# Performance work log

Hardware: AMD Instinct MI355X
Metric: run time of the kernel (lower is better)

## Reference

```python
import jax, jax.numpy as jnp
import numpy as np

B, C, H, W = 8, 256, 128, 128
K = 3                      # kernel_size
GC = 16                    # group_channels
G = C // GC                # groups = 16
RED = 4                    # reduction_ratio (hardcoded in module)
CR = C // RED              # 64
PAD = (K - 1) // 2


def setup_inputs() -> dict:
    key = jax.random.key(0)
    ks = jax.random.split(key, 8)
    s = 0.05
    return {
        "x":  jax.random.normal(ks[0], (B, C, H, W), dtype=jnp.float32),
        # conv1[0]: 1x1 Conv2d(C, C//4)
        "w1": jax.random.normal(ks[1], (CR, C), dtype=jnp.float32) * s,
        "b1": jax.random.normal(ks[2], (CR,), dtype=jnp.float32) * s,
        # conv1[1]: depthwise KxK Conv2d(C//4, C//4, groups=C//4), padding=K//2
        "wd": jax.random.normal(ks[3], (CR, 1, K, K), dtype=jnp.float32) * s,
        "bd": jax.random.normal(ks[4], (CR,), dtype=jnp.float32) * s,
        # conv2: 1x1 Conv2d(C//4, K*K*G)
        "w2": jax.random.normal(ks[5], (K * K * G, CR), dtype=jnp.float32) * s,
        "b2": jax.random.normal(ks[6], (K * K * G,), dtype=jnp.float32) * s,
    }


def _forward(x, w1, b1, wd, bd, w2, b2):
    # weight generation branch: 1x1 conv -> depthwise KxK conv -> 1x1 conv
    y = jnp.einsum("oc,bchw->bohw", w1, x) + b1[None, :, None, None]
    y = jax.lax.conv_general_dilated(
        y, wd, window_strides=(1, 1),
        padding=[(PAD, PAD), (PAD, PAD)],
        feature_group_count=CR,
        dimension_numbers=("NCHW", "OIHW", "NCHW"),
    ) + bd[None, :, None, None]
    w = jnp.einsum("oc,bchw->bohw", w2, y) + b2[None, :, None, None]
    w = w.reshape(B, G, K, K, H, W)  # per-pixel dynamic depthwise weights

    # involution-style per-pixel depthwise conv, stride=1, padding=(K-1)//2
    xr = x.reshape(B, G, GC, H, W)
    xp = jnp.pad(xr, ((0, 0), (0, 0), (0, 0), (PAD, PAD), (PAD, PAD)))
    out = jnp.zeros((B, G, GC, H, W), dtype=x.dtype)
    for kh in range(K):          # small fixed structural loop (K*K = 9 taps)
        for kw in range(K):
            out = out + xp[:, :, :, kh:kh + H, kw:kw + W] * w[:, :, kh, kw][:, :, None, :, :]
    return out.reshape(B, C, H, W)


def reference(x, w1, b1, wd, bd, w2, b2):
    return _forward(x, w1, b1, wd, bd, w2, b2)
```

## Files before the change

kernel.cpp:

```cpp
#include <hip/hip_runtime.h>
#include <hip/hip_bf16.h>

#define HW    16384
#define IMW   128
#define IMH   128
#define CIN   256
#define CR    64
#define G     16
#define GC    16

typedef __attribute__((ext_vector_type(8))) short short8;
typedef __attribute__((ext_vector_type(4))) float floatx4;

static __device__ __forceinline__ short f2bf(float f) {
  union { float f; unsigned u; } v; v.f = f;
  unsigned r = v.u + 0x7fffu + ((v.u >> 16) & 1u);
  return (short)(r >> 16);
}
static __device__ __forceinline__ float bf2f(short s) {
  union { unsigned u; float f; } v; v.u = ((unsigned)(unsigned short)s) << 16;
  return v.f;
}

__global__ __launch_bounds__(256) void k_cvt_w1(const float* __restrict__ w1,
                                                short* __restrict__ w1b) {
  const int i = blockIdx.x * 256 + threadIdx.x;
  w1b[i] = f2bf(w1[i]);
}

__global__ __launch_bounds__(256) void k_conv1_mfma(const float* __restrict__ x,
                                                    const short* __restrict__ w1b,
                                                    const float* __restrict__ b1,
                                                    short* __restrict__ y1b) {
  const int blk  = blockIdx.x;
  const int b    = blk >> 8;
  const int pt   = blk & 255;
  const int wave = threadIdx.x >> 6;
  const int lane = threadIdx.x & 63;
  const int quad = lane >> 4;
  const int l16  = lane & 15;
  const int p    = pt * 64 + wave * 16 + l16;

  const float* xb = x + (size_t)b * CIN * HW + p;

  floatx4 acc[4];
#pragma unroll
  for (int mt = 0; mt < 4; ++mt)
#pragma unroll
    for (int r = 0; r < 4; ++r) acc[mt][r] = b1[mt * 16 + quad * 4 + r];

#pragma unroll 1
  for (int kk = 0; kk < CIN; kk += 64) {
    short8 af0[4], af1[4];
#pragma unroll
    for (int mt = 0; mt < 4; ++mt) {
      af0[mt] = *(const short8*)(w1b + (mt * 16 + l16) * CIN + kk + quad * 8);
      af1[mt] = *(const short8*)(w1b + (mt * 16 + l16) * CIN + kk + 32 + quad * 8);
    }
    float xv0[8], xv1[8];
#pragma unroll
    for (int j = 0; j < 8; ++j)
      xv0[j] = xb[(size_t)(kk + quad * 8 + j) * HW];
#pragma unroll
    for (int j = 0; j < 8; ++j)
      xv1[j] = xb[(size_t)(kk + 32 + quad * 8 + j) * HW];

    short8 bf0, bf1;
#pragma unroll
    for (int j = 0; j < 8; ++j) bf0[j] = f2bf(xv0[j]);
#pragma unroll
    for (int j = 0; j < 8; ++j) bf1[j] = f2bf(xv1[j]);

#pragma unroll
    for (int mt = 0; mt < 4; ++mt)
      acc[mt] = __builtin_amdgcn_mfma_f32_16x16x32_bf16(af0[mt], bf0, acc[mt], 0, 0, 0);
#pragma unroll
    for (int mt = 0; mt < 4; ++mt)
      acc[mt] = __builtin_amdgcn_mfma_f32_16x16x32_bf16(af1[mt], bf1, acc[mt], 0, 0, 0);
  }

  short* yb = y1b + (size_t)b * CR * HW + p;
#pragma unroll
  for (int mt = 0; mt < 4; ++mt)
#pragma unroll
    for (int r = 0; r < 4; ++r)
      yb[(size_t)(mt * 16 + quad * 4 + r) * HW] = f2bf(acc[mt][r]);
}

__global__ __launch_bounds__(256) void k_dw(const short* __restrict__ y1b,
                                            const float* __restrict__ wd,
                                            const float* __restrict__ bd,
                                            short* __restrict__ y2b) {
  const int blk   = blockIdx.x;
  const int strip = blk & 3;
  const int c     = (blk >> 2) & 63;
  const int b     = blk >> 8;
  const int tcol  = threadIdx.x & 15;
  const int trow  = threadIdx.x >> 4;
  const int r0    = strip * 32 + trow * 2;
  const int c0    = tcol * 8;

  const short* src = y1b + (size_t)(b * CR + c) * HW;

  const float mcl = c0 > 0 ? 1.f : 0.f;
  const float mcr = c0 + 8 < IMW ? 1.f : 0.f;
  const int   cl  = c0 > 0 ? c0 - 1 : 0;
  const int   crr = c0 + 8 < IMW ? c0 + 8 : IMW - 1;

  float f[4][10];
#pragma unroll
  for (int i = 0; i < 4; ++i) {
    const int rr = r0 - 1 + i;
    const int rc = rr < 0 ? 0 : (rr > IMH - 1 ? IMH - 1 : rr);
    const float mr = (rr < 0 || rr > IMH - 1) ? 0.f : 1.f;
    const short* row = src + rc * IMW;
    const short8 v = *(const short8*)(row + c0);
#pragma unroll
    for (int j = 0; j < 8; ++j) f[i][j + 1] = mr * bf2f(v[j]);
    f[i][0] = mr * mcl * bf2f(row[cl]);
    f[i][9] = mr * mcr * bf2f(row[crr]);
  }

  float wv[9];
#pragma unroll
  for (int j = 0; j < 9; ++j) wv[j] = wd[c * 9 + j];
  const float bias = bd[c];

  short* dst = y2b + (size_t)(b * CR + c) * HW + r0 * IMW + c0;
#pragma unroll
  for (int i = 0; i < 2; ++i) {
    short8 o;
#pragma unroll
    for (int xcol = 0; xcol < 8; ++xcol) {
      float acc = bias;
#pragma unroll
      for (int kh = 0; kh < 3; ++kh)
#pragma unroll
        for (int kw = 0; kw < 3; ++kw)
          acc += wv[kh * 3 + kw] * f[i + kh][xcol + kw];
      o[xcol] = f2bf(acc);
    }
    *(short8*)(dst + i * IMW) = o;
  }
}

__global__ __launch_bounds__(256) void k_conv2invol(const float* __restrict__ x,
                                                    const short* __restrict__ y2b,
                                                    const float* __restrict__ w2,
                                                    const float* __restrict__ b2,
                                                    float* __restrict__ out) {
  const int blk  = blockIdx.x;
  const int tile = blk & 63;
  const int gp   = (blk >> 6) & 7;
  const int b    = blk >> 9;
  const int g0   = gp * 2;
  const int tid  = threadIdx.x;
  const int tr   = tid >> 5;
  const int tc   = tid & 31;
  const int h    = (tile >> 2) * 8 + tr;
  const int w    = (tile & 3) * 32 + tc;
  const int p    = h * IMW + w;

  float wv[2][9];
#pragma unroll
  for (int q = 0; q < 2; ++q)
#pragma unroll
    for (int j = 0; j < 9; ++j) wv[q][j] = b2[(g0 + q) * 9 + j];

  const short* y2p = y2b + (size_t)b * CR * HW + p;
#pragma unroll 2
  for (int c = 0; c < CR; c += 4) {
    const float v0 = bf2f(y2p[(size_t)(c + 0) * HW]);
    const float v1 = bf2f(y2p[(size_t)(c + 1) * HW]);
    const float v2 = bf2f(y2p[(size_t)(c + 2) * HW]);
    const float v3 = bf2f(y2p[(size_t)(c + 3) * HW]);
#pragma unroll
    for (int q = 0; q < 2; ++q)
#pragma unroll
      for (int j = 0; j < 9; ++j) {
        const float4 wq = *(const float4*)(w2 + ((g0 + q) * 9 + j) * CR + c);
        wv[q][j] += wq.x * v0 + wq.y * v1 + wq.z * v2 + wq.w * v3;
      }
  }

  const int   hcl[3] = {h > 0 ? h - 1 : 0, h, h < IMH - 1 ? h + 1 : IMH - 1};
  const int   wcl[3] = {w > 0 ? w - 1 : 0, w, w < IMW - 1 ? w + 1 : IMW - 1};
  const float mr[3]  = {h > 0 ? 1.f : 0.f, 1.f, h < IMH - 1 ? 1.f : 0.f};
  const float mc[3]  = {w > 0 ? 1.f : 0.f, 1.f, w < IMW - 1 ? 1.f : 0.f};
  int rel[9];
#pragma unroll
  for (int kh = 0; kh < 3; ++kh)
#pragma unroll
    for (int kw = 0; kw < 3; ++kw) {
      rel[kh * 3 + kw] = hcl[kh] * IMW + wcl[kw];
      const float m = mr[kh] * mc[kw];
      wv[0][kh * 3 + kw] *= m;
      wv[1][kh * 3 + kw] *= m;
    }

  const float* xb = x + (size_t)b * CIN * HW;
  float*       ob = out + (size_t)b * CIN * HW;

#pragma unroll
  for (int q = 0; q < 2; ++q) {
#pragma unroll 4
    for (int cc = 0; cc < GC; ++cc) {
      const int ch = (g0 + q) * GC + cc;
      const float* xp = xb + (size_t)ch * HW;
      float acc = 0.f;
#pragma unroll
      for (int j = 0; j < 9; ++j) acc += wv[q][j] * xp[rel[j]];
      ob[(size_t)ch * HW + p] = acc;
    }
  }
}

extern "C" void kernel_launch(void* const* d_in, const int* in_sizes, int n_in,
                              void* d_out, int out_size, void* d_ws, size_t ws_size,
                              hipStream_t stream) {
  const float* x  = (const float*)d_in[0];
  const float* w1 = (const float*)d_in[1];
  const float* b1 = (const float*)d_in[2];
  const float* wd = (const float*)d_in[3];
  const float* bd = (const float*)d_in[4];
  const float* w2 = (const float*)d_in[5];
  const float* b2 = (const float*)d_in[6];
  float* out = (float*)d_out;

  short* w1b = (short*)d_ws;
  short* y1b = (short*)((char*)d_ws + 65536);
  short* y2b = y1b + (size_t)8 * CR * HW;

  k_cvt_w1<<<dim3(64), dim3(256), 0, stream>>>(w1, w1b);
  k_conv1_mfma<<<dim3(2048), dim3(256), 0, stream>>>(x, w1b, b1, y1b);
  k_dw<<<dim3(2048), dim3(256), 0, stream>>>(y1b, wd, bd, y2b);
  k_conv2invol<<<dim3(4096), dim3(256), 0, stream>>>(x, y2b, w2, b2, out);
}
```

Measured before the change: 353.3 us.

## Generate involution weights with split-bf16 MFMA and vectorize the involution stage

The per-pixel weight generation (the conv2 1x1 projection) now runs on bf16 MFMA instead of scalar FMAs. w2 is split into a high and a residual bf16 part to keep accuracy close to fp32. Each block computes 144x64 weights into shared memory and then applies the 3x3 involution to all 16 groups for a 64-pixel row segment, with each thread handling 4 contiguous pixels through float4 loads and stores. This removes the redundant weight recomputation the old layout did per group pair and cuts scalar load traffic. In exchange it doubles the MFMA count and adds shared memory and a barrier per block. The bf16 w1 buffer is now aliased onto the y2 buffer, which is safe only because conv1 finishes reading it before the depthwise kernel writes y2.

```diff
diff --git a/kernel.cpp b/kernel.cpp
--- a/kernel.cpp
+++ b/kernel.cpp
@@ -8,6 +8,7 @@
 #define CR    64
 #define G     16
 #define GC    16
+#define M2    144
 
 typedef __attribute__((ext_vector_type(8))) short short8;
 typedef __attribute__((ext_vector_type(4))) float floatx4;
@@ -22,10 +23,22 @@
   return v.f;
 }
 
-__global__ __launch_bounds__(256) void k_cvt_w1(const float* __restrict__ w1,
-                                                short* __restrict__ w1b) {
-  const int i = blockIdx.x * 256 + threadIdx.x;
-  w1b[i] = f2bf(w1[i]);
+__global__ __launch_bounds__(256) void k_cvt(const float* __restrict__ w1,
+                                             const float* __restrict__ w2,
+                                             short* __restrict__ w1b,
+                                             short* __restrict__ w2b,
+                                             short* __restrict__ w2r) {
+  const int blk = blockIdx.x;
+  if (blk < 64) {
+    const int i = blk * 256 + threadIdx.x;
+    w1b[i] = f2bf(w1[i]);
+  } else {
+    const int i = (blk - 64) * 256 + threadIdx.x;
+    const float v = w2[i];
+    const short hb = f2bf(v);
+    w2b[i] = hb;
+    w2r[i] = f2bf(v - bf2f(hb));
+  }
 }
 
 __global__ __launch_bounds__(256) void k_conv1_mfma(const float* __restrict__ x,
@@ -144,74 +157,116 @@
   }
 }
 
-__global__ __launch_bounds__(256) void k_conv2invol(const float* __restrict__ x,
+__global__ __launch_bounds__(256) void k_wgen_invol(const float* __restrict__ x,
                                                     const short* __restrict__ y2b,
-                                                    const float* __restrict__ w2,
+                                                    const short* __restrict__ w2b,
+                                                    const short* __restrict__ w2r,
                                                     const float* __restrict__ b2,
                                                     float* __restrict__ out) {
+  __shared__ float wgt[M2 * 64];
   const int blk  = blockIdx.x;
-  const int tile = blk & 63;
-  const int gp   = (blk >> 6) & 7;
-  const int b    = blk >> 9;
-  const int g0   = gp * 2;
+  const int b    = blk >> 8;
+  const int pt   = blk & 255;
   const int tid  = threadIdx.x;
-  const int tr   = tid >> 5;
-  const int tc   = tid & 31;
-  const int h    = (tile >> 2) * 8 + tr;
-  const int w    = (tile & 3) * 32 + tc;
-  const int p    = h * IMW + w;
-
-  float wv[2][9];
-#pragma unroll
-  for (int q = 0; q < 2; ++q)
-#pragma unroll
-    for (int j = 0; j < 9; ++j) wv[q][j] = b2[(g0 + q) * 9 + j];
-
-  const short* y2p = y2b + (size_t)b * CR * HW + p;
+  const int wave = tid >> 6;
+  const int lane = tid & 63;
+  const int quad = lane >> 4;
+  const int l16  = lane & 15;
+
+  {
+    const int p = pt * 64 + wave * 16 + l16;
+    const short* y2p = y2b + (size_t)b * CR * HW + p;
+
+    floatx4 acc[9];
+#pragma unroll
+    for (int mt = 0; mt < 9; ++mt)
+#pragma unroll
+      for (int r = 0; r < 4; ++r) acc[mt][r] = b2[mt * 16 + quad * 4 + r];
+
+#pragma unroll
+    for (int kk = 0; kk < CR; kk += 32) {
+      short8 bfrag;
+#pragma unroll
+      for (int j = 0; j < 8; ++j)
+        bfrag[j] = y2p[(size_t)(kk + quad * 8 + j) * HW];
+#pragma unroll
+      for (int mt = 0; mt < 9; ++mt) {
+        const short8 af = *(const short8*)(w2b + (mt * 16 + l16) * CR + kk + quad * 8);
+        acc[mt] = __builtin_amdgcn_mfma_f32_16x16x32_bf16(af, bfrag, acc[mt], 0, 0, 0);
+      }
+#pragma unroll
+      for (int mt = 0; mt < 9; ++mt) {
+        const short8 ar = *(const short8*)(w2r + (mt * 16 + l16) * CR + kk + quad * 8);
+        acc[mt] = __builtin_amdgcn_mfma_f32_16x16x32_bf16(ar, bfrag, acc[mt], 0, 0, 0);
+      }
+    }
+
+#pragma unroll
+    for (int mt = 0; mt < 9; ++mt)
+#pragma unroll
+      for (int r = 0; r < 4; ++r)
+        wgt[(mt * 16 + quad * 4 + r) * 64 + wave * 16 + l16] = acc[mt][r];
+  }
+  __syncthreads();
+
+  const int pq  = tid & 15;
+  const int g   = tid >> 4;
+  const int h   = pt >> 1;
+  const int c0q = (pt & 1) * 64 + pq * 4;
+  const int p0  = h * IMW + c0q;
+
+  float wv[9][4];
+#pragma unroll
+  for (int j = 0; j < 9; ++j) {
+    const float4 v = *(const float4*)&wgt[(g * 9 + j) * 64 + pq * 4];
+    wv[j][0] = v.x; wv[j][1] = v.y; wv[j][2] = v.z; wv[j][3] = v.w;
+  }
+
+  if (h == 0) {
+#pragma unroll
+    for (int j = 0; j < 3; ++j)
+      wv[j][0] = wv[j][1] = wv[j][2] = wv[j][3] = 0.f;
+  }
+  if (h == IMH - 1) {
+#pragma unroll
+    for (int j = 6; j < 9; ++j)
+      wv[j][0] = wv[j][1] = wv[j][2] = wv[j][3] = 0.f;
+  }
+  if (c0q == 0)       { wv[0][0] = wv[3][0] = wv[6][0] = 0.f; }
+  if (c0q == IMW - 4) { wv[2][3] = wv[5][3] = wv[8][3] = 0.f; }
+
+  const int r[3] = { (h > 0 ? h - 1 : 0) * IMW, h * IMW,
+                     (h < IMH - 1 ? h + 1 : IMH - 1) * IMW };
+  const int cl = c0q > 0 ? c0q - 1 : 0;
+  const int cr = c0q + 4 < IMW ? c0q + 4 : IMW - 1;
+
+  const float* xg = x   + ((size_t)b * CIN + (size_t)g * GC) * HW;
+  float*       og = out + ((size_t)b * CIN + (size_t)g * GC) * HW;
+
 #pragma unroll 2
-  for (int c = 0; c < CR; c += 4) {
-    const float v0 = bf2f(y2p[(size_t)(c + 0) * HW]);
-    const float v1 = bf2f(y2p[(size_t)(c + 1) * HW]);
-    const float v2 = bf2f(y2p[(size_t)(c + 2) * HW]);
-    const float v3 = bf2f(y2p[(size_t)(c + 3) * HW]);
-#pragma unroll
-    for (int q = 0; q < 2; ++q)
-#pragma unroll
-      for (int j = 0; j < 9; ++j) {
-        const float4 wq = *(const float4*)(w2 + ((g0 + q) * 9 + j) * CR + c);
-        wv[q][j] += wq.x * v0 + wq.y * v1 + wq.z * v2 + wq.w * v3;
-      }
-  }
-
-  const int   hcl[3] = {h > 0 ? h - 1 : 0, h, h < IMH - 1 ? h + 1 : IMH - 1};
-  const int   wcl[3] = {w > 0 ? w - 1 : 0, w, w < IMW - 1 ? w + 1 : IMW - 1};
-  const float mr[3]  = {h > 0 ? 1.f : 0.f, 1.f, h < IMH - 1 ? 1.f : 0.f};
-  const float mc[3]  = {w > 0 ? 1.f : 0.f, 1.f, w < IMW - 1 ? 1.f : 0.f};
-  int rel[9];
-#pragma unroll
-  for (int kh = 0; kh < 3; ++kh)
-#pragma unroll
-    for (int kw = 0; kw < 3; ++kw) {
-      rel[kh * 3 + kw] = hcl[kh] * IMW + wcl[kw];
-      const float m = mr[kh] * mc[kw];
-      wv[0][kh * 3 + kw] *= m;
-      wv[1][kh * 3 + kw] *= m;
-    }
-
-  const float* xb = x + (size_t)b * CIN * HW;
-  float*       ob = out + (size_t)b * CIN * HW;
-
-#pragma unroll
-  for (int q = 0; q < 2; ++q) {
-#pragma unroll 4
-    for (int cc = 0; cc < GC; ++cc) {
-      const int ch = (g0 + q) * GC + cc;
-      const float* xp = xb + (size_t)ch * HW;
+  for (int cc = 0; cc < GC; ++cc) {
+    const float* xp = xg + (size_t)cc * HW;
+    float v[3][6];
+#pragma unroll
+    for (int rr = 0; rr < 3; ++rr) {
+      const float4 m = *(const float4*)(xp + r[rr] + c0q);
+      v[rr][0] = xp[r[rr] + cl];
+      v[rr][1] = m.x; v[rr][2] = m.y; v[rr][3] = m.z; v[rr][4] = m.w;
+      v[rr][5] = xp[r[rr] + cr];
+    }
+    float o[4];
+#pragma unroll
+    for (int px = 0; px < 4; ++px) {
       float acc = 0.f;
 #pragma unroll
-      for (int j = 0; j < 9; ++j) acc += wv[q][j] * xp[rel[j]];
-      ob[(size_t)ch * HW + p] = acc;
-    }
+      for (int kh = 0; kh < 3; ++kh)
+#pragma unroll
+        for (int kw = 0; kw < 3; ++kw)
+          acc += wv[kh * 3 + kw][px] * v[kh][px + kw];
+      o[px] = acc;
+    }
+    float4 ov; ov.x = o[0]; ov.y = o[1]; ov.z = o[2]; ov.w = o[3];
+    *(float4*)(og + (size_t)cc * HW + p0) = ov;
   }
 }
 
@@ -227,12 +282,14 @@
   const float* b2 = (const float*)d_in[6];
   float* out = (float*)d_out;
 
-  short* w1b = (short*)d_ws;
-  short* y1b = (short*)((char*)d_ws + 65536);
-  short* y2b = y1b + (size_t)8 * CR * HW;
-
-  k_cvt_w1<<<dim3(64), dim3(256), 0, stream>>>(w1, w1b);
+  short* w2b = (short*)d_ws;
+  short* w2r = (short*)((char*)d_ws + 18432);
+  short* y1b = (short*)((char*)d_ws + 36864);
+  short* y2b = (short*)((char*)d_ws + 16814080);
+  short* w1b = y2b;
+
+  k_cvt<<<dim3(100), dim3(256), 0, stream>>>(w1, w2, w1b, w2b, w2r);
   k_conv1_mfma<<<dim3(2048), dim3(256), 0, stream>>>(x, w1b, b1, y1b);
   k_dw<<<dim3(2048), dim3(256), 0, stream>>>(y1b, wd, bd, y2b);
-  k_conv2invol<<<dim3(4096), dim3(256), 0, stream>>>(x, y2b, w2, b2, out);
-}
+  k_wgen_invol<<<dim3(2048), dim3(256), 0, stream>>>(x, y2b, w2b, w2r, b2, out);
+}
```

New measurement: 403.4 us. 14.2% more time.

## Compute conv2 dynamic weights with bf16 MFMA using split hi/lo weights

Applied to the files above, without the earlier changes.

Replaces the scalar FMA loop that produced the 18 per-pixel involution weights with bf16 MFMA tiles. w2 is pre-packed into a padded bf16 high part plus a bf16 residual so precision stays close to fp32. Results go through shared memory to the per-pixel involution stage. This removes redundant w2 loads and scalar FMAs, at the cost of a __syncthreads, 18KB of LDS per block, wasted MFMA rows from padding 18 to 32, and uncoalesced short gathers of y2b. w1b now aliases the y2b workspace region, which is safe because it is consumed by conv1 before k_dw writes y2b.

```diff
diff --git a/kernel.cpp b/kernel.cpp
--- a/kernel.cpp
+++ b/kernel.cpp
@@ -22,10 +22,25 @@
   return v.f;
 }
 
-__global__ __launch_bounds__(256) void k_cvt_w1(const float* __restrict__ w1,
-                                                short* __restrict__ w1b) {
-  const int i = blockIdx.x * 256 + threadIdx.x;
-  w1b[i] = f2bf(w1[i]);
+__global__ __launch_bounds__(256) void k_cvt(const float* __restrict__ w1,
+                                             const float* __restrict__ w2,
+                                             short* __restrict__ w1b,
+                                             short* __restrict__ w2p,
+                                             short* __restrict__ w2pr) {
+  const int blk = blockIdx.x;
+  const int tid = threadIdx.x;
+  if (blk < 64) {
+    const int i = blk * 256 + tid;
+    w1b[i] = f2bf(w1[i]);
+  } else {
+    const int idx  = (blk & 63) * 256 + tid;
+    const int gp   = idx >> 11;
+    const int mrow = (idx >> 6) & 31;
+    const int c    = idx & 63;
+    const float val = mrow < 18 ? w2[(gp * 18 + mrow) * 64 + c] : 0.f;
+    if (blk < 128) w2p[idx]  = f2bf(val);
+    else           w2pr[idx] = f2bf(val - bf2f(f2bf(val)));
+  }
 }
 
 __global__ __launch_bounds__(256) void k_conv1_mfma(const float* __restrict__ x,
@@ -146,42 +161,92 @@
 
 __global__ __launch_bounds__(256) void k_conv2invol(const float* __restrict__ x,
                                                     const short* __restrict__ y2b,
-                                                    const float* __restrict__ w2,
+                                                    const short* __restrict__ w2p,
+                                                    const short* __restrict__ w2pr,
                                                     const float* __restrict__ b2,
                                                     float* __restrict__ out) {
+  __shared__ float wgt[18 * 256];
   const int blk  = blockIdx.x;
   const int tile = blk & 63;
   const int gp   = (blk >> 6) & 7;
   const int b    = blk >> 9;
   const int g0   = gp * 2;
   const int tid  = threadIdx.x;
-  const int tr   = tid >> 5;
-  const int tc   = tid & 31;
-  const int h    = (tile >> 2) * 8 + tr;
-  const int w    = (tile & 3) * 32 + tc;
-  const int p    = h * IMW + w;
+  const int wave = tid >> 6;
+  const int lane = tid & 63;
+  const int quad = lane >> 4;
+  const int l16  = lane & 15;
+  const int h0   = (tile >> 2) * 8;
+  const int w0   = (tile & 3) * 32;
+
+  {
+    const short* y2base = y2b + (size_t)b * CR * HW;
+    int pabs[4];
+#pragma unroll
+    for (int t = 0; t < 4; ++t)
+      pabs[t] = (h0 + 2 * wave + (t >> 1)) * IMW + w0 + (t & 1) * 16 + l16;
+
+    floatx4 acc[2][4];
+#pragma unroll
+    for (int mt = 0; mt < 2; ++mt)
+#pragma unroll
+      for (int t = 0; t < 4; ++t)
+#pragma unroll
+        for (int r = 0; r < 4; ++r) {
+          const int row = mt * 16 + quad * 4 + r;
+          acc[mt][t][r] = row < 18 ? b2[gp * 18 + row] : 0.f;
+        }
+
+#pragma unroll
+    for (int kk = 0; kk < CR; kk += 32) {
+      short8 bfrag[4];
+#pragma unroll
+      for (int t = 0; t < 4; ++t)
+#pragma unroll
+        for (int j = 0; j < 8; ++j)
+          bfrag[t][j] = y2base[(size_t)(kk + quad * 8 + j) * HW + pabs[t]];
+#pragma unroll
+      for (int mt = 0; mt < 2; ++mt) {
+        const short8 am = *(const short8*)(w2p + (gp * 32 + mt * 16 + l16) * 64 + kk + quad * 8);
+#pragma unroll
+        for (int t = 0; t < 4; ++t)
+          acc[mt][t] = __builtin_amdgcn_mfma_f32_16x16x32_bf16(am, bfrag[t], acc[mt][t], 0, 0, 0);
+      }
+#pragma unroll
+      for (int mt = 0; mt < 2; ++mt) {
+        const short8 ar = *(const short8*)(w2pr + (gp * 32 + mt * 16 + l16) * 64 + kk + quad * 8);
+#pragma unroll
+        for (int t = 0; t < 4; ++t)
+          acc[mt][t] = __builtin_amdgcn_mfma_f32_16x16x32_bf16(ar, bfrag[t], acc[mt][t], 0, 0, 0);
+      }
+    }
+
+#pragma unroll
+    for (int mt = 0; mt < 2; ++mt)
+#pragma unroll
+      for (int t = 0; t < 4; ++t) {
+        const int pxl = (2 * wave + (t >> 1)) * 32 + (t & 1) * 16 + l16;
+#pragma unroll
+        for (int r = 0; r < 4; ++r) {
+          const int row = mt * 16 + quad * 4 + r;
+          if (row < 18) wgt[row * 256 + pxl] = acc[mt][t][r];
+        }
+      }
+  }
+  __syncthreads();
+
+  const int tr = tid >> 5;
+  const int tc = tid & 31;
+  const int h  = h0 + tr;
+  const int w  = w0 + tc;
+  const int p  = h * IMW + w;
 
   float wv[2][9];
 #pragma unroll
   for (int q = 0; q < 2; ++q)
 #pragma unroll
-    for (int j = 0; j < 9; ++j) wv[q][j] = b2[(g0 + q) * 9 + j];
-
-  const short* y2p = y2b + (size_t)b * CR * HW + p;
-#pragma unroll 2
-  for (int c = 0; c < CR; c += 4) {
-    const float v0 = bf2f(y2p[(size_t)(c + 0) * HW]);
-    const float v1 = bf2f(y2p[(size_t)(c + 1) * HW]);
-    const float v2 = bf2f(y2p[(size_t)(c + 2) * HW]);
-    const float v3 = bf2f(y2p[(size_t)(c + 3) * HW]);
-#pragma unroll
-    for (int q = 0; q < 2; ++q)
-#pragma unroll
-      for (int j = 0; j < 9; ++j) {
-        const float4 wq = *(const float4*)(w2 + ((g0 + q) * 9 + j) * CR + c);
-        wv[q][j] += wq.x * v0 + wq.y * v1 + wq.z * v2 + wq.w * v3;
-      }
-  }
+    for (int j = 0; j < 9; ++j)
+      wv[q][j] = wgt[(q * 9 + j) * 256 + tid];
 
   const int   hcl[3] = {h > 0 ? h - 1 : 0, h, h < IMH - 1 ? h + 1 : IMH - 1};
   const int   wcl[3] = {w > 0 ? w - 1 : 0, w, w < IMW - 1 ? w + 1 : IMW - 1};
@@ -227,12 +292,14 @@
   const float* b2 = (const float*)d_in[6];
   float* out = (float*)d_out;
 
-  short* w1b = (short*)d_ws;
-  short* y1b = (short*)((char*)d_ws + 65536);
-  short* y2b = y1b + (size_t)8 * CR * HW;
-
-  k_cvt_w1<<<dim3(64), dim3(256), 0, stream>>>(w1, w1b);
+  short* w2p  = (short*)d_ws;
+  short* w2pr = (short*)((char*)d_ws + 32768);
+  short* y1b  = (short*)((char*)d_ws + 65536);
+  short* y2b  = (short*)((char*)d_ws + 65536 + 16777216);
+  short* w1b  = y2b;
+
+  k_cvt<<<dim3(192), dim3(256), 0, stream>>>(w1, w2, w1b, w2p, w2pr);
   k_conv1_mfma<<<dim3(2048), dim3(256), 0, stream>>>(x, w1b, b1, y1b);
   k_dw<<<dim3(2048), dim3(256), 0, stream>>>(y1b, wd, bd, y2b);
-  k_conv2invol<<<dim3(4096), dim3(256), 0, stream>>>(x, y2b, w2, b2, out);
-}
+  k_conv2invol<<<dim3(4096), dim3(256), 0, stream>>>(x, y2b, w2p, w2pr, b2, out);
+}
```

Result: slower. 386.8 us (+9.5%).
